# Optimization experiments

Measured on AMD Instinct MI355X. Metric: run time of the kernel, lower is better.

The kernel has to match this reference:

```python
import jax, jax.numpy as jnp
import numpy as np

D = 512   # dim (number of groups)
H = 8192  # h = dim * v
U = 64    # u
V = H // D  # 16
N = 4096  # batch
EPS = 1e-12  # torch F.normalize eps


def setup_inputs() -> dict:
    key = jax.random.key(0)
    k_x, k_w1, k_b1, k_w2, k_b2 = jax.random.split(key, 5)
    x = jax.random.normal(k_x, (N, H), dtype=jnp.float32)
    # grouped Conv1d(dim*v, dim*u, k=1, groups=dim) == per-group [u, v] matmul
    s1 = 1.0 / np.sqrt(V)
    W1 = jax.random.uniform(k_w1, (D, U, V), jnp.float32, -s1, s1)
    b1 = jax.random.uniform(k_b1, (D, U), jnp.float32, -s1, s1)
    # grouped Conv1d(dim*u, dim, k=1, groups=dim) == per-group [1, u] matmul
    s2 = 1.0 / np.sqrt(U)
    W2 = jax.random.uniform(k_w2, (D, U), jnp.float32, -s2, s2)
    b2 = jax.random.uniform(k_b2, (D,), jnp.float32, -s2, s2)
    return {"x": x, "W1": W1, "b1": b1, "W2": W2, "b2": b2}


def reference(x, W1, b1, W2, b2):
    # x: [N, H] -> [N, D, V] (channel layout of Conv1d groups)
    xg = x.reshape(-1, D, V)
    # grouped 1x1 conv #1: per-group v -> u matmul, + bias
    h1 = jnp.einsum('ndv,duv->ndu', xg, W1) + b1  # [N, D, U]
    h1 = jax.nn.elu(h1)
    # grouped 1x1 conv #2: per-group u -> 1 matmul, + bias
    y = jnp.einsum('ndu,du->nd', h1, W2) + b2  # [N, D]
    # L2 normalize (torch F.normalize semantics: x / max(||x||, eps))
    nrm = jnp.sqrt(jnp.sum(y * y, axis=-1, keepdims=True))
    return y / jnp.maximum(nrm, EPS)
```

## Files before the change

kernel.cpp:

```cpp
#include <hip/hip_runtime.h>
#include <math.h>

#define D_ 512
#define H_ 8192
#define U_ 64
#define V_ 16
#define N_ 4096
#define DUV (D_ * U_ * V_)

#define BR 64
#define BG 8
#define XSTR (BG * V_ + 4)
#define YSTR 12

typedef __bf16 bf16x8 __attribute__((ext_vector_type(8)));
typedef __bf16 bf16x4 __attribute__((ext_vector_type(4)));
typedef float f32x4 __attribute__((ext_vector_type(4)));

__global__ __launch_bounds__(256) void k0_split_w1(const float* __restrict__ W1,
                                                   __bf16* __restrict__ wh) {
    __bf16* wl = wh + DUV;
    const int i4 = (blockIdx.x * 256 + threadIdx.x) * 4;
    f32x4 w = *(const f32x4*)(W1 + i4);
    bf16x4 h, l;
    #pragma unroll
    for (int j = 0; j < 4; ++j) {
        float wf = w[j];
        __bf16 hh = (__bf16)wf;
        h[j] = hh;
        l[j] = (__bf16)(wf - (float)hh);
    }
    *(bf16x4*)(wh + i4) = h;
    *(bf16x4*)(wl + i4) = l;
}

template <bool PRESPLIT>
__global__ __launch_bounds__(256, 4) void k1_div_encoder(
        const float* __restrict__ x,
        const float* __restrict__ W1,
        const __bf16* __restrict__ wsplit,
        const float* __restrict__ b1,
        const float* __restrict__ W2,
        const float* __restrict__ b2,
        float* __restrict__ y) {
    __shared__ float xs[BR][XSTR];
    __shared__ float ytile[BR][YSTR];

    const int tid  = threadIdx.x;
    const int lane = tid & 63;
    const int wave = __builtin_amdgcn_readfirstlane(tid >> 6);
    const int q    = lane >> 4;
    const int m    = lane & 15;
    const int vbase = (q & 1) * 8;

    const int nb = blockIdx.x & 63;
    const int db = blockIdx.x >> 6;
    const int r0 = nb * BR;
    const int d0 = db * BG;

    {
        const float* xg = x + (size_t)r0 * H_ + (size_t)d0 * V_;
        #pragma unroll
        for (int i = 0; i < 8; ++i) {
            const int flat = tid + i * 256;
            const int row  = flat >> 5;
            const int c4   = flat & 31;
            f32x4 v = *(const f32x4*)(xg + (size_t)row * H_ + c4 * 4);
            *(f32x4*)&xs[row][c4 * 4] = v;
        }
    }
    __syncthreads();

    #pragma unroll 1
    for (int gi = 0; gi < 2; ++gi) {
        const int gl = wave * 2 + gi;
        const int d  = d0 + gl;

        bf16x8 Afrag[4];
        if (PRESPLIT) {
            const __bf16* base = wsplit + (size_t)(q >> 1) * DUV;
            #pragma unroll
            for (int c = 0; c < 4; ++c) {
                Afrag[c] = *(const bf16x8*)(base +
                    ((size_t)d * U_ + c * 16 + m) * V_ + vbase);
            }
        } else {
            #pragma unroll
            for (int c = 0; c < 4; ++c) {
                const float* wp = W1 + ((size_t)d * U_ + c * 16 + m) * V_ + vbase;
                f32x4 w0 = *(const f32x4*)wp;
                f32x4 w1v = *(const f32x4*)(wp + 4);
                float wf[8] = {w0.x, w0.y, w0.z, w0.w, w1v.x, w1v.y, w1v.z, w1v.w};
                bf16x8 a;
                #pragma unroll
                for (int i = 0; i < 8; ++i) {
                    __bf16 h = (__bf16)wf[i];
                    __bf16 l = (__bf16)(wf[i] - (float)h);
                    a[i] = (q < 2) ? h : l;
                }
                Afrag[c] = a;
            }
        }

        f32x4 b1frag[4], w2frag[4];
        #pragma unroll
        for (int c = 0; c < 4; ++c) {
            b1frag[c] = *(const f32x4*)(b1 + (size_t)d * U_ + c * 16 + q * 4);
            w2frag[c] = *(const f32x4*)(W2 + (size_t)d * U_ + c * 16 + q * 4);
        }
        const float b2s = b2[d];

        #pragma unroll 2
        for (int t = 0; t < 4; ++t) {
            const float* bp = &xs[t * 16 + m][gl * V_ + vbase];
            f32x4 x0 = *(const f32x4*)bp;
            f32x4 x1 = *(const f32x4*)(bp + 4);
            float xf[8] = {x0.x, x0.y, x0.z, x0.w, x1.x, x1.y, x1.z, x1.w};
            bf16x8 bhi, blo;
            #pragma unroll
            for (int i = 0; i < 8; ++i) {
                __bf16 h = (__bf16)xf[i];
                bhi[i] = h;
                blo[i] = (__bf16)(xf[i] - (float)h);
            }

            float partial = 0.0f;
            #pragma unroll
            for (int c = 0; c < 4; ++c) {
                f32x4 acc = b1frag[c];
                acc = __builtin_amdgcn_mfma_f32_16x16x32_bf16(Afrag[c], bhi, acc, 0, 0, 0);
                acc = __builtin_amdgcn_mfma_f32_16x16x32_bf16(Afrag[c], blo, acc, 0, 0, 0);
                #pragma unroll
                for (int r = 0; r < 4; ++r) {
                    float h = acc[r];
                    float e = fmaxf(h, __expf(fminf(h, 0.0f)) - 1.0f);
                    partial = fmaf(w2frag[c][r], e, partial);
                }
            }
            partial += __shfl_xor(partial, 16, 64);
            partial += __shfl_xor(partial, 32, 64);
            if (q == 0) {
                ytile[t * 16 + m][gl] = partial + b2s;
            }
        }
    }
    __syncthreads();

    if (tid < 128) {
        const int row  = tid >> 1;
        const int half = tid & 1;
        f32x4 v = *(const f32x4*)&ytile[row][half * 4];
        *(f32x4*)(y + (size_t)(r0 + row) * D_ + d0 + half * 4) = v;
    }
}

__global__ __launch_bounds__(256) void k2_l2_normalize(float* __restrict__ y) {
    const int n = blockIdx.x;
    const int t = threadIdx.x;
    float* row = y + (size_t)n * D_;

    float v0 = row[t];
    float v1 = row[t + 256];
    float ss = v0 * v0 + v1 * v1;

    #pragma unroll
    for (int off = 32; off > 0; off >>= 1) {
        ss += __shfl_down(ss, off, 64);
    }

    __shared__ float wsum[4];
    if ((t & 63) == 0) wsum[t >> 6] = ss;
    __syncthreads();
    const float tot = wsum[0] + wsum[1] + wsum[2] + wsum[3];

    const float scale = 1.0f / fmaxf(sqrtf(tot), 1e-12f);

    row[t]       = v0 * scale;
    row[t + 256] = v1 * scale;
}

extern "C" void kernel_launch(void* const* d_in, const int* in_sizes, int n_in,
                              void* d_out, int out_size, void* d_ws, size_t ws_size,
                              hipStream_t stream) {
    const float* x  = (const float*)d_in[0];
    const float* W1 = (const float*)d_in[1];
    const float* b1 = (const float*)d_in[2];
    const float* W2 = (const float*)d_in[3];
    const float* b2 = (const float*)d_in[4];
    float* y = (float*)d_out;

    const dim3 grid((N_ / BR) * (D_ / BG));
    if (ws_size >= (size_t)(2 * DUV * sizeof(__bf16))) {
        __bf16* wh = (__bf16*)d_ws;
        k0_split_w1<<<dim3(DUV / 4 / 256), dim3(256), 0, stream>>>(W1, wh);
        k1_div_encoder<true><<<grid, dim3(256), 0, stream>>>(
            x, W1, wh, b1, W2, b2, y);
    } else {
        k1_div_encoder<false><<<grid, dim3(256), 0, stream>>>(
            x, W1, (const __bf16*)nullptr, b1, W2, b2, y);
    }
    k2_l2_normalize<<<dim3(N_), dim3(256), 0, stream>>>(y);
}
```

Baseline: 221.4 us.

## Give each wave one group over 512 rows, streaming x from registers with prefetch

```diff
diff --git a/kernel.cpp b/kernel.cpp
--- a/kernel.cpp
+++ b/kernel.cpp
@@ -8,9 +8,9 @@
 #define N_ 4096
 #define DUV (D_ * U_ * V_)
 
-#define BR 64
 #define BG 8
-#define XSTR (BG * V_ + 4)
+#define RB 512
+#define NI (RB / 16)
 #define YSTR 12
 
 typedef __bf16 bf16x8 __attribute__((ext_vector_type(8)));
@@ -35,7 +35,7 @@
 }
 
 template <bool PRESPLIT>
-__global__ __launch_bounds__(256, 4) void k1_div_encoder(
+__global__ __launch_bounds__(512, 4) void k1_div_encoder(
         const float* __restrict__ x,
         const float* __restrict__ W1,
         const __bf16* __restrict__ wsplit,
@@ -43,8 +43,7 @@
         const float* __restrict__ W2,
         const float* __restrict__ b2,
         float* __restrict__ y) {
-    __shared__ float xs[BR][XSTR];
-    __shared__ float ytile[BR][YSTR];
+    __shared__ float yt[RB][YSTR];
 
     const int tid  = threadIdx.x;
     const int lane = tid & 63;
@@ -53,104 +52,98 @@
     const int m    = lane & 15;
     const int vbase = (q & 1) * 8;
 
-    const int nb = blockIdx.x & 63;
-    const int db = blockIdx.x >> 6;
-    const int r0 = nb * BR;
+    const int db = blockIdx.x & 63;
+    const int nb = blockIdx.x >> 6;
     const int d0 = db * BG;
+    const int d  = d0 + wave;
+    const int r0 = nb * RB;
 
-    {
-        const float* xg = x + (size_t)r0 * H_ + (size_t)d0 * V_;
+    bf16x8 Af[4];
+    f32x4  b1f[4], w2f[4];
+    if (PRESPLIT) {
+        const __bf16* base = wsplit + (size_t)(q >> 1) * DUV;
+        #pragma unroll
+        for (int c = 0; c < 4; ++c) {
+            Af[c] = *(const bf16x8*)(base +
+                ((size_t)d * U_ + c * 16 + m) * V_ + vbase);
+        }
+    } else {
+        #pragma unroll
+        for (int c = 0; c < 4; ++c) {
+            const float* wp = W1 + ((size_t)d * U_ + c * 16 + m) * V_ + vbase;
+            f32x4 w0 = *(const f32x4*)wp;
+            f32x4 w1v = *(const f32x4*)(wp + 4);
+            float wf[8] = {w0.x, w0.y, w0.z, w0.w, w1v.x, w1v.y, w1v.z, w1v.w};
+            bf16x8 a;
+            #pragma unroll
+            for (int i = 0; i < 8; ++i) {
+                __bf16 h = (__bf16)wf[i];
+                __bf16 l = (__bf16)(wf[i] - (float)h);
+                a[i] = (q < 2) ? h : l;
+            }
+            Af[c] = a;
+        }
+    }
+    #pragma unroll
+    for (int c = 0; c < 4; ++c) {
+        b1f[c] = *(const f32x4*)(b1 + (size_t)d * U_ + c * 16 + q * 4);
+        w2f[c] = *(const f32x4*)(W2 + (size_t)d * U_ + c * 16 + q * 4);
+    }
+    const float b2s = b2[d];
+
+    const float* lp = x + (size_t)(r0 + m) * H_ + d * V_ + vbase;
+
+    f32x4 c0 = *(const f32x4*)lp;
+    f32x4 c1 = *(const f32x4*)(lp + 4);
+    lp += (size_t)16 * H_;
+
+    #pragma unroll 2
+    for (int it = 0; it < NI; ++it) {
+        f32x4 n0 = {}, n1 = {};
+        if (it + 1 < NI) {
+            n0 = *(const f32x4*)lp;
+            n1 = *(const f32x4*)(lp + 4);
+            lp += (size_t)16 * H_;
+        }
+
+        float xf[8] = {c0.x, c0.y, c0.z, c0.w, c1.x, c1.y, c1.z, c1.w};
+        bf16x8 bhi, blo;
         #pragma unroll
         for (int i = 0; i < 8; ++i) {
-            const int flat = tid + i * 256;
-            const int row  = flat >> 5;
-            const int c4   = flat & 31;
-            f32x4 v = *(const f32x4*)(xg + (size_t)row * H_ + c4 * 4);
-            *(f32x4*)&xs[row][c4 * 4] = v;
+            __bf16 h = (__bf16)xf[i];
+            bhi[i] = h;
+            blo[i] = (__bf16)(xf[i] - (float)h);
         }
+
+        float partial = 0.0f;
+        #pragma unroll
+        for (int c = 0; c < 4; ++c) {
+            f32x4 acc = b1f[c];
+            acc = __builtin_amdgcn_mfma_f32_16x16x32_bf16(Af[c], bhi, acc, 0, 0, 0);
+            acc = __builtin_amdgcn_mfma_f32_16x16x32_bf16(Af[c], blo, acc, 0, 0, 0);
+            #pragma unroll
+            for (int r = 0; r < 4; ++r) {
+                float h = acc[r];
+                float e = fmaxf(h, __expf(fminf(h, 0.0f)) - 1.0f);
+                partial = fmaf(w2f[c][r], e, partial);
+            }
+        }
+        partial += __shfl_xor(partial, 16, 64);
+        partial += __shfl_xor(partial, 32, 64);
+        if (q == 0) {
+            yt[it * 16 + m][wave] = partial + b2s;
+        }
+        c0 = n0;
+        c1 = n1;
     }
     __syncthreads();
 
-    #pragma unroll 1
-    for (int gi = 0; gi < 2; ++gi) {
-        const int gl = wave * 2 + gi;
-        const int d  = d0 + gl;
-
-        bf16x8 Afrag[4];
-        if (PRESPLIT) {
-            const __bf16* base = wsplit + (size_t)(q >> 1) * DUV;
-            #pragma unroll
-            for (int c = 0; c < 4; ++c) {
-                Afrag[c] = *(const bf16x8*)(base +
-                    ((size_t)d * U_ + c * 16 + m) * V_ + vbase);
-            }
-        } else {
-            #pragma unroll
-            for (int c = 0; c < 4; ++c) {
-                const float* wp = W1 + ((size_t)d * U_ + c * 16 + m) * V_ + vbase;
-                f32x4 w0 = *(const f32x4*)wp;
-                f32x4 w1v = *(const f32x4*)(wp + 4);
-                float wf[8] = {w0.x, w0.y, w0.z, w0.w, w1v.x, w1v.y, w1v.z, w1v.w};
-                bf16x8 a;
-                #pragma unroll
-                for (int i = 0; i < 8; ++i) {
-                    __bf16 h = (__bf16)wf[i];
-                    __bf16 l = (__bf16)(wf[i] - (float)h);
-                    a[i] = (q < 2) ? h : l;
-                }
-                Afrag[c] = a;
-            }
-        }
-
-        f32x4 b1frag[4], w2frag[4];
-        #pragma unroll
-        for (int c = 0; c < 4; ++c) {
-            b1frag[c] = *(const f32x4*)(b1 + (size_t)d * U_ + c * 16 + q * 4);
-            w2frag[c] = *(const f32x4*)(W2 + (size_t)d * U_ + c * 16 + q * 4);
-        }
-        const float b2s = b2[d];
-
-        #pragma unroll 2
-        for (int t = 0; t < 4; ++t) {
-            const float* bp = &xs[t * 16 + m][gl * V_ + vbase];
-            f32x4 x0 = *(const f32x4*)bp;
-            f32x4 x1 = *(const f32x4*)(bp + 4);
-            float xf[8] = {x0.x, x0.y, x0.z, x0.w, x1.x, x1.y, x1.z, x1.w};
-            bf16x8 bhi, blo;
-            #pragma unroll
-            for (int i = 0; i < 8; ++i) {
-                __bf16 h = (__bf16)xf[i];
-                bhi[i] = h;
-                blo[i] = (__bf16)(xf[i] - (float)h);
-            }
-
-            float partial = 0.0f;
-            #pragma unroll
-            for (int c = 0; c < 4; ++c) {
-                f32x4 acc = b1frag[c];
-                acc = __builtin_amdgcn_mfma_f32_16x16x32_bf16(Afrag[c], bhi, acc, 0, 0, 0);
-                acc = __builtin_amdgcn_mfma_f32_16x16x32_bf16(Afrag[c], blo, acc, 0, 0, 0);
-                #pragma unroll
-                for (int r = 0; r < 4; ++r) {
-                    float h = acc[r];
-                    float e = fmaxf(h, __expf(fminf(h, 0.0f)) - 1.0f);
-                    partial = fmaf(w2frag[c][r], e, partial);
-                }
-            }
-            partial += __shfl_xor(partial, 16, 64);
-            partial += __shfl_xor(partial, 32, 64);
-            if (q == 0) {
-                ytile[t * 16 + m][gl] = partial + b2s;
-            }
-        }
-    }
-    __syncthreads();
-
-    if (tid < 128) {
-        const int row  = tid >> 1;
-        const int half = tid & 1;
-        f32x4 v = *(const f32x4*)&ytile[row][half * 4];
-        *(f32x4*)(y + (size_t)(r0 + row) * D_ + d0 + half * 4) = v;
+    {
+        f32x4 v0 = *(const f32x4*)&yt[tid][0];
+        f32x4 v1 = *(const f32x4*)&yt[tid][4];
+        float* yp = y + (size_t)(r0 + tid) * D_ + d0;
+        *(f32x4*)yp = v0;
+        *(f32x4*)(yp + 4) = v1;
     }
 }
 
@@ -189,14 +182,14 @@
     const float* b2 = (const float*)d_in[4];
     float* y = (float*)d_out;
 
-    const dim3 grid((N_ / BR) * (D_ / BG));
+    const dim3 grid((N_ / RB) * (D_ / BG));
     if (ws_size >= (size_t)(2 * DUV * sizeof(__bf16))) {
         __bf16* wh = (__bf16*)d_ws;
         k0_split_w1<<<dim3(DUV / 4 / 256), dim3(256), 0, stream>>>(W1, wh);
-        k1_div_encoder<true><<<grid, dim3(256), 0, stream>>>(
+        k1_div_encoder<true><<<grid, dim3(512), 0, stream>>>(
             x, W1, wh, b1, W2, b2, y);
     } else {
-        k1_div_encoder<false><<<grid, dim3(256), 0, stream>>>(
+        k1_div_encoder<false><<<grid, dim3(512), 0, stream>>>(
             x, W1, (const __bf16*)nullptr, b1, W2, b2, y);
     }
     k2_l2_normalize<<<dim3(N_), dim3(256), 0, stream>>>(y);
```

Result: no change. 217.3 us (-1.8%).
